# Performance work log

Hardware: AMD Instinct MI355X
Metric: run time of the kernel (lower is better)

The kernel has to match this reference:

```python
import jax, jax.numpy as jnp
import numpy as np

D_MODEL = 1024
NUM_HEADS = 16
D_K = D_MODEL // NUM_HEADS
B, L = 2, 4096


def setup_inputs() -> dict:
    key = jax.random.key(0)
    ks = jax.random.split(key, 12)
    s = 0.02
    return {
        "q": jax.random.normal(ks[0], (B, L, D_MODEL), dtype=jnp.float32),
        "k": jax.random.normal(ks[1], (B, L, D_MODEL), dtype=jnp.float32),
        "v": jax.random.normal(ks[2], (B, L, D_MODEL), dtype=jnp.float32),
        "Wq": jax.random.normal(ks[3], (D_MODEL, D_MODEL), dtype=jnp.float32) * s,
        "bq": jax.random.normal(ks[4], (D_MODEL,), dtype=jnp.float32) * s,
        "Wk": jax.random.normal(ks[5], (D_MODEL, D_MODEL), dtype=jnp.float32) * s,
        "bk": jax.random.normal(ks[6], (D_MODEL,), dtype=jnp.float32) * s,
        "Wv": jax.random.normal(ks[7], (D_MODEL, D_MODEL), dtype=jnp.float32) * s,
        "bv": jax.random.normal(ks[8], (D_MODEL,), dtype=jnp.float32) * s,
        "Wo": jax.random.normal(ks[9], (D_MODEL, D_MODEL), dtype=jnp.float32) * s,
        "bo": jax.random.normal(ks[10], (D_MODEL,), dtype=jnp.float32) * s,
    }


def reference(q, k, v, Wq, bq, Wk, bk, Wv, bv, Wo, bo):
    b, l, _ = q.shape
    # projections (torch Linear: x @ W.T + b), reshape to [b, l, h, d]
    qf = (q @ Wq.T + bq).reshape(b, l, NUM_HEADS, D_K)
    kf = (k @ Wk.T + bk).reshape(b, l, NUM_HEADS, D_K)
    vf = (v @ Wv.T + bv).reshape(b, l, NUM_HEADS, D_K)
    # elu+1 feature map (positive features)
    qf = jax.nn.elu(qf) + 1.0
    kf = jax.nn.elu(kf) + 1.0
    # normalizer uses full-sequence k sum (as in the original code)
    z = 1.0 / (jnp.einsum("blhd,bhd->blh", qf, kf.sum(axis=1)) + 1e-6)
    # cumulative sums over sequence (the linear-attention scan state)
    k_cum = jnp.cumsum(kf, axis=1)  # [b, l, h, d]
    v_cum = jnp.cumsum(vf, axis=1)  # [b, l, h, d]
    context = jnp.einsum("blhd,blhd->blh", qf, k_cum)  # [b, l, h]
    context = context[..., None] * v_cum * z[..., None]  # [b, l, h, d]
    context = context.reshape(b, l, NUM_HEADS * D_K)
    return context @ Wo.T + bo
```

## Files before the change

kernel.cpp:

```cpp
#include <hip/hip_runtime.h>
#include <hip/hip_bf16.h>
#include <cstdint>
#include <cstddef>

#define D_MODEL 1024
#define NUM_HEADS 16
#define DK_DIM 64
#define BATCH 2
#define SEQ 4096
#define MROWS (BATCH*SEQ)
#define NCHUNK 128
#define CHUNK 32

#define BM 256
#define BN 128
#define BK 64
#define NSLOT 3
#define SLOT_SH (BM*BK + BN*BK)
#define KTILES (D_MODEL/BK)

typedef __attribute__((ext_vector_type(4))) float f32x4;
typedef __attribute__((ext_vector_type(2))) float f32x2;
typedef __attribute__((ext_vector_type(8))) short bf16x8;
typedef __attribute__((ext_vector_type(4))) short s16x4;
typedef __attribute__((ext_vector_type(2))) uint32_t u32x2;
typedef __attribute__((ext_vector_type(4))) uint32_t u32x4;

__device__ __forceinline__ float b2f(short s) {
  union { uint32_t u; float f; } c; c.u = ((uint32_t)(uint16_t)s) << 16; return c.f;
}
__device__ __forceinline__ short f2b(float f) {
  union { float f; uint32_t u; } c; c.f = f;
  uint32_t u = c.u;
  u += 0x7FFFu + ((u >> 16) & 1u);
  return (short)(u >> 16);
}
__device__ __forceinline__ f32x4 b4_to_f4(s16x4 s) {
  f32x4 r;
  r.x = b2f(s.x); r.y = b2f(s.y); r.z = b2f(s.z); r.w = b2f(s.w);
  return r;
}
__device__ __forceinline__ uint32_t cvtpk(float lo, float hi) {
  uint32_t r;
  asm("v_cvt_pk_bf16_f32 %0, %1, %2" : "=v"(r) : "v"(lo), "v"(hi));
  return r;
}

__global__ __launch_bounds__(256) void cvt_w4(
    const float* __restrict__ s0, const float* __restrict__ s1,
    const float* __restrict__ s2, const float* __restrict__ s3,
    short* __restrict__ dst) {
  const int y = blockIdx.y;
  const float* s = (y == 0) ? s0 : (y == 1) ? s1 : (y == 2) ? s2 : s3;
  const int i = blockIdx.x * 256 + threadIdx.x;
  float4 v = reinterpret_cast<const float4*>(s)[i];
  s16x4 o;
  o.x = f2b(v.x); o.y = f2b(v.y); o.z = f2b(v.z); o.w = f2b(v.w);
  reinterpret_cast<s16x4*>(dst)[(size_t)y * (D_MODEL * D_MODEL / 4) + i] = o;
}

template<int AFP32, int OUTBF16, int CSUM>
__global__ __launch_bounds__(512, 2) void gemm8(
    const void* __restrict__ A0, const void* __restrict__ A1,
    const void* __restrict__ A2, const short* __restrict__ Wbase,
    const float* __restrict__ b0, const float* __restrict__ b1,
    const float* __restrict__ b2, void* __restrict__ Cbase, int actmask,
    float* __restrict__ ckp, float* __restrict__ cvp)
{
  extern __shared__ __align__(16) short lds[];
  const int tid = threadIdx.x;
  const int wid = tid >> 6;
  const int lane = tid & 63;
  const int brow = blockIdx.x * BM;
  const int bcol = blockIdx.y * BN;
  const int z = blockIdx.z;
  const int wr = wid >> 1, wc = wid & 1;

  const void* Ap = (z == 0) ? A0 : (z == 1) ? A1 : A2;
  const float* bias = (z == 0) ? b0 : (z == 1) ? b1 : b2;
  const short* Bw = Wbase + (size_t)z * D_MODEL * D_MODEL;
  const int act = (actmask >> z) & 1;
  const float* __restrict__ A32 = (const float*)Ap;
  const short* __restrict__ A16 = (const short*)Ap;

  f32x4 acc[4][4];
#pragma unroll
  for (int i = 0; i < 4; ++i)
#pragma unroll
    for (int j = 0; j < 4; ++j)
#pragma unroll
      for (int t = 0; t < 4; ++t) acc[i][j][t] = 0.f;

  const int srow = lane >> 3;
  const int gql  = lane & 7;
  const int sgel = (gql ^ srow) * 8;

  auto stageB = [&](int t) {
    short* sB = lds + (t % NSLOT) * SLOT_SH + BM * BK;
    const int k0 = t * BK;
#pragma unroll
    for (int i = 0; i < 2; ++i) {
      const int r = i * 64 + wid * 8;
      const short* g = Bw + (size_t)(bcol + r + srow) * D_MODEL + k0 + sgel;
      __builtin_amdgcn_global_load_lds((const __attribute__((address_space(1))) void*)g,
          (__attribute__((address_space(3))) void*)(sB + r * BK), 16, 0, 0);
    }
  };
  auto stageA16 = [&](int t) {
    short* sA = lds + (t % NSLOT) * SLOT_SH;
    const int k0 = t * BK;
#pragma unroll
    for (int i = 0; i < 4; ++i) {
      const int r = i * 64 + wid * 8;
      const short* g = A16 + (size_t)(brow + r + srow) * D_MODEL + k0 + sgel;
      __builtin_amdgcn_global_load_lds((const __attribute__((address_space(1))) void*)g,
          (__attribute__((address_space(3))) void*)(sA + r * BK), 16, 0, 0);
    }
  };
  auto loadA32 = [&](int t, float4 (&buf)[8]) {
    const int k0 = t * BK;
#pragma unroll
    for (int i = 0; i < 4; ++i) {
      const float* src = A32 + (size_t)(brow + i * 64 + wid * 8 + srow) * D_MODEL + k0 + gql * 8;
      buf[2 * i]     = *reinterpret_cast<const float4*>(src);
      buf[2 * i + 1] = *reinterpret_cast<const float4*>(src + 4);
    }
  };
  auto writeA32 = [&](int t, float4 (&buf)[8]) {
    char* sA = (char*)(lds + (t % NSLOT) * SLOT_SH);
#pragma unroll
    for (int i = 0; i < 4; ++i) {
      u32x4 w;
      w.x = cvtpk(buf[2 * i].x,     buf[2 * i].y);
      w.y = cvtpk(buf[2 * i].z,     buf[2 * i].w);
      w.z = cvtpk(buf[2 * i + 1].x, buf[2 * i + 1].y);
      w.w = cvtpk(buf[2 * i + 1].z, buf[2 * i + 1].w);
      const int ebyte = (i * 64 + wid * 8 + srow) * 128 + ((gql ^ srow) * 16);
      *reinterpret_cast<u32x4*>(sA + ebyte) = w;
    }
  };

  const int lane15 = lane & 15;
  const int swz = (lane & 7) << 4;
  const int kq = (lane >> 4) * 16;

  auto compute = [&](int t) {
    const char* sAb = (const char*)(lds + (t % NSLOT) * SLOT_SH);
    const char* sBb = sAb + BM * BK * 2;
    auto rdA = [&](int mi, int ks) -> bf16x8 {
      const int row = wr * 64 + mi * 16 + lane15;
      const int off = row * 128 + ((ks * 64 + kq) ^ swz);
      return *reinterpret_cast<const bf16x8*>(sAb + off);
    };
    auto rdB = [&](int nj, int ks) -> bf16x8 {
      const int row = wc * 64 + nj * 16 + lane15;
      const int off = row * 128 + ((ks * 64 + kq) ^ swz);
      return *reinterpret_cast<const bf16x8*>(sBb + off);
    };
    bf16x8 Af[2][2], Bf[2][2][2];
#pragma unroll
    for (int m2 = 0; m2 < 2; ++m2)
#pragma unroll
      for (int ks = 0; ks < 2; ++ks) Af[m2][ks] = rdA(m2, ks);
#pragma unroll
    for (int j2 = 0; j2 < 2; ++j2)
#pragma unroll
      for (int ks = 0; ks < 2; ++ks) Bf[0][j2][ks] = rdB(j2, ks);
#pragma unroll
    for (int m2 = 0; m2 < 2; ++m2)
#pragma unroll
      for (int j2 = 0; j2 < 2; ++j2)
#pragma unroll
        for (int ks = 0; ks < 2; ++ks)
          acc[m2][j2] = __builtin_amdgcn_mfma_f32_16x16x32_bf16(Bf[0][j2][ks], Af[m2][ks], acc[m2][j2], 0, 0, 0);
#pragma unroll
    for (int j2 = 0; j2 < 2; ++j2)
#pragma unroll
      for (int ks = 0; ks < 2; ++ks) Bf[1][j2][ks] = rdB(2 + j2, ks);
#pragma unroll
    for (int m2 = 0; m2 < 2; ++m2)
#pragma unroll
      for (int j2 = 0; j2 < 2; ++j2)
#pragma unroll
        for (int ks = 0; ks < 2; ++ks)
          acc[m2][2 + j2] = __builtin_amdgcn_mfma_f32_16x16x32_bf16(Bf[1][j2][ks], Af[m2][ks], acc[m2][2 + j2], 0, 0, 0);
#pragma unroll
    for (int m2 = 0; m2 < 2; ++m2)
#pragma unroll
      for (int ks = 0; ks < 2; ++ks) Af[m2][ks] = rdA(2 + m2, ks);
#pragma unroll
    for (int m2 = 0; m2 < 2; ++m2)
#pragma unroll
      for (int j2 = 0; j2 < 2; ++j2)
#pragma unroll
        for (int ks = 0; ks < 2; ++ks)
          acc[2 + m2][2 + j2] = __builtin_amdgcn_mfma_f32_16x16x32_bf16(Bf[1][j2][ks], Af[m2][ks], acc[2 + m2][2 + j2], 0, 0, 0);
#pragma unroll
    for (int m2 = 0; m2 < 2; ++m2)
#pragma unroll
      for (int j2 = 0; j2 < 2; ++j2)
#pragma unroll
        for (int ks = 0; ks < 2; ++ks)
          acc[2 + m2][j2] = __builtin_amdgcn_mfma_f32_16x16x32_bf16(Bf[0][j2][ks], Af[m2][ks], acc[2 + m2][j2], 0, 0, 0);
  };

  if constexpr (AFP32) {
    float4 buf0[8], buf1[8];
    loadA32(0, buf0);
    asm volatile("s_waitcnt vmcnt(0)" ::: "memory");
    writeA32(0, buf0);
    loadA32(1, buf1);
    stageB(0); stageB(1);

    auto body = [&](int t, float4 (&bufW)[8], float4 (&bufL)[8]) {
      if (t == KTILES - 1) { asm volatile("s_waitcnt vmcnt(0)" ::: "memory"); }
      else                 { asm volatile("s_waitcnt vmcnt(2)" ::: "memory"); }
      if (t + 1 < KTILES) writeA32(t + 1, bufW);
      if (t + 2 < KTILES) loadA32(t + 2, bufL);
      asm volatile("s_waitcnt lgkmcnt(0)" ::: "memory");
      __builtin_amdgcn_s_barrier();
      __builtin_amdgcn_sched_barrier(0);
      if (t + 2 < KTILES) stageB(t + 2);
      compute(t);
    };
#pragma unroll 1
    for (int t2 = 0; t2 < KTILES; t2 += 2) {
      body(t2,     buf1, buf0);
      body(t2 + 1, buf0, buf1);
    }
  } else {
    stageA16(0); stageB(0);
    stageA16(1); stageB(1);
#pragma unroll 1
    for (int t = 0; t < KTILES; ++t) {
      if (t == KTILES - 1) { asm volatile("s_waitcnt vmcnt(0)" ::: "memory"); }
      else                 { asm volatile("s_waitcnt vmcnt(6)" ::: "memory"); }
      __builtin_amdgcn_s_barrier();
      __builtin_amdgcn_sched_barrier(0);
      if (t + 2 < KTILES) { stageA16(t + 2); stageB(t + 2); }
      compute(t);
    }
  }

  const int csub4 = (lane >> 4) * 4;
  f32x4 csum[2][4];
  if constexpr (CSUM) {
#pragma unroll
    for (int cp = 0; cp < 2; ++cp)
#pragma unroll
      for (int nj = 0; nj < 4; ++nj)
#pragma unroll
        for (int t = 0; t < 4; ++t) csum[cp][nj][t] = 0.f;
  }
#pragma unroll
  for (int mi = 0; mi < 4; ++mi) {
    const int row = brow + wr * 64 + mi * 16 + lane15;
    const size_t rowbase = (size_t)z * MROWS * D_MODEL + (size_t)row * D_MODEL;
#pragma unroll
    for (int nj = 0; nj < 4; ++nj) {
      const int col0 = bcol + wc * 64 + nj * 16 + csub4;
      const float4 bv = *reinterpret_cast<const float4*>(&bias[col0]);
      float v0 = acc[mi][nj][0] + bv.x;
      float v1 = acc[mi][nj][1] + bv.y;
      float v2 = acc[mi][nj][2] + bv.z;
      float v3 = acc[mi][nj][3] + bv.w;
      if (act) {
        v0 = (v0 > 0.f) ? (v0 + 1.f) : __expf(v0);
        v1 = (v1 > 0.f) ? (v1 + 1.f) : __expf(v1);
        v2 = (v2 > 0.f) ? (v2 + 1.f) : __expf(v2);
        v3 = (v3 > 0.f) ? (v3 + 1.f) : __expf(v3);
      }
      if constexpr (CSUM) {
        csum[mi >> 1][nj][0] += v0;
        csum[mi >> 1][nj][1] += v1;
        csum[mi >> 1][nj][2] += v2;
        csum[mi >> 1][nj][3] += v3;
      }
      if (OUTBF16) {
        u32x2 w;
        w.x = cvtpk(v0, v1);
        w.y = cvtpk(v2, v3);
        *reinterpret_cast<u32x2*>(&((short*)Cbase)[rowbase + col0]) = w;
      } else {
        float4 w; w.x = v0; w.y = v1; w.z = v2; w.w = v3;
        *reinterpret_cast<float4*>(&((float*)Cbase)[rowbase + col0]) = w;
      }
    }
  }
  if constexpr (CSUM) {
    if (z >= 1) {
      float* dst = (z == 1) ? ckp : cvp;
      const int b  = brow >> 12;
      const int l0 = brow & (SEQ - 1);
      const int h  = (bcol >> 6) + wc;
      const int bh = b * NUM_HEADS + h;
#pragma unroll
      for (int cp = 0; cp < 2; ++cp) {
#pragma unroll
        for (int nj = 0; nj < 4; ++nj) {
          f32x4 s = csum[cp][nj];
#pragma unroll
          for (int m = 1; m < 16; m <<= 1) {
            s[0] += __shfl_xor(s[0], m, 64);
            s[1] += __shfl_xor(s[1], m, 64);
            s[2] += __shfl_xor(s[2], m, 64);
            s[3] += __shfl_xor(s[3], m, 64);
          }
          if (lane15 == 0) {
            const int cg = (l0 >> 5) + wr * 2 + cp;
            const int d0 = nj * 16 + csub4;
            *reinterpret_cast<f32x4*>(
                &dst[((size_t)(bh * NCHUNK + cg)) * DK_DIM + d0]) = s;
          }
        }
      }
    }
  }
}

__global__ __launch_bounds__(256) void chunk_scan(
    float* __restrict__ ck, float* __restrict__ cv, float* __restrict__ ksum)
{
  __shared__ float sk[4][64], sv[4][64];
  const int bh = blockIdx.x;
  const int tid = threadIdx.x;
  const int d = tid & 63;
  const int g = tid >> 6;
  const int c0 = g * 32;

  float rk = 0.f, rv = 0.f;
#pragma unroll 4
  for (int c = c0; c < c0 + 32; ++c) {
    const size_t o = ((size_t)(bh * NCHUNK + c)) * DK_DIM + d;
    rk += ck[o]; rv += cv[o];
  }
  sk[g][d] = rk; sv[g][d] = rv;
  __syncthreads();
  float runk = 0.f, runv = 0.f;
  for (int gg = 0; gg < g; ++gg) { runk += sk[gg][d]; runv += sv[gg][d]; }
#pragma unroll 4
  for (int c = c0; c < c0 + 32; ++c) {
    const size_t o = ((size_t)(bh * NCHUNK + c)) * DK_DIM + d;
    const float tk = ck[o], tv = cv[o];
    ck[o] = runk; cv[o] = runv;
    runk += tk; runv += tv;
  }
  if (g == 3) ksum[bh * DK_DIM + d] = runk;
}

__global__ __launch_bounds__(256) void scan_ctx(
    const short* __restrict__ qf, const short* __restrict__ kf,
    const short* __restrict__ vf,
    const float* __restrict__ ck, const float* __restrict__ cv,
    const float* __restrict__ ksum, short* __restrict__ ctx)
{
  const int gw = blockIdx.x * 4 + (threadIdx.x >> 6);
  const int lane = threadIdx.x & 63;
  const int pg = lane >> 4;
  const int dg = lane & 15;
  const int c = gw & (NCHUNK - 1);
  const int h = (gw >> 7) & (NUM_HEADS - 1);
  const int b = gw >> 11;
  const int bh = b * NUM_HEADS + h;
  const int d4 = dg * 4;

  f32x4 krun = *reinterpret_cast<const f32x4*>(
      &ck[((size_t)(bh * NCHUNK + c)) * DK_DIM + d4]);
  f32x4 vrun = *reinterpret_cast<const f32x4*>(
      &cv[((size_t)(bh * NCHUNK + c)) * DK_DIM + d4]);
  const f32x4 kst = *reinterpret_cast<const f32x4*>(&ksum[bh * DK_DIM + d4]);

  const size_t base = ((size_t)(b * SEQ + c * CHUNK) * NUM_HEADS + h) * DK_DIM + d4;

  for (int p0 = 0; p0 < CHUNK; p0 += 4) {
    const size_t qoff = base + (size_t)(p0 + pg) * D_MODEL;
    const f32x4 q4 = b4_to_f4(*reinterpret_cast<const s16x4*>(&qf[qoff]));
    f32x4 sk, sv;
#pragma unroll
    for (int i = 0; i < 4; ++i) {
      const size_t off = base + (size_t)(p0 + i) * D_MODEL;
      krun += b4_to_f4(*reinterpret_cast<const s16x4*>(&kf[off]));
      vrun += b4_to_f4(*reinterpret_cast<const s16x4*>(&vf[off]));
      if (i == pg) { sk = krun; sv = vrun; }
    }
    float s1 = q4.x * sk.x + q4.y * sk.y + q4.z * sk.z + q4.w * sk.w;
    float s2 = q4.x * kst.x + q4.y * kst.y + q4.z * kst.z + q4.w * kst.w;
#pragma unroll
    for (int m = 1; m < 16; m <<= 1) {
      s1 += __shfl_xor(s1, m, 64);
      s2 += __shfl_xor(s2, m, 64);
    }
    const float g = s1 / (s2 + 1e-6f);
    s16x4 o;
    o.x = f2b(g * sv.x); o.y = f2b(g * sv.y);
    o.z = f2b(g * sv.z); o.w = f2b(g * sv.w);
    *reinterpret_cast<s16x4*>(&ctx[qoff]) = o;
  }
}

extern "C" void kernel_launch(void* const* d_in, const int* in_sizes, int n_in,
                              void* d_out, int out_size, void* d_ws, size_t ws_size,
                              hipStream_t stream) {
  const float* q  = (const float*)d_in[0];
  const float* k  = (const float*)d_in[1];
  const float* v  = (const float*)d_in[2];
  const float* Wq = (const float*)d_in[3];
  const float* bq = (const float*)d_in[4];
  const float* Wk = (const float*)d_in[5];
  const float* bk = (const float*)d_in[6];
  const float* Wv = (const float*)d_in[7];
  const float* bv = (const float*)d_in[8];
  const float* Wo = (const float*)d_in[9];
  const float* bo = (const float*)d_in[10];
  float* out = (float*)d_out;

  uint8_t* p = (uint8_t*)d_ws;
  auto alloc = [&](size_t bytes) { uint8_t* r = p; p += bytes; return r; };
  short* qf  = (short*)alloc((size_t)MROWS * D_MODEL * 2);
  short* kf  = (short*)alloc((size_t)MROWS * D_MODEL * 2);
  short* vf  = (short*)alloc((size_t)MROWS * D_MODEL * 2);
  short* ctx = (short*)alloc((size_t)MROWS * D_MODEL * 2);
  short* Wqb = (short*)alloc((size_t)D_MODEL * D_MODEL * 2);
  short* Wkb = (short*)alloc((size_t)D_MODEL * D_MODEL * 2);
  short* Wvb = (short*)alloc((size_t)D_MODEL * D_MODEL * 2);
  short* Wob = (short*)alloc((size_t)D_MODEL * D_MODEL * 2);
  float* ck   = (float*)alloc((size_t)BATCH * NUM_HEADS * NCHUNK * DK_DIM * 4);
  float* cv   = (float*)alloc((size_t)BATCH * NUM_HEADS * NCHUNK * DK_DIM * 4);
  float* ksum = (float*)alloc((size_t)BATCH * NUM_HEADS * DK_DIM * 4);
  (void)Wkb; (void)Wvb;

  const dim3 gproj(MROWS / BM, D_MODEL / BN, 3);
  const dim3 gout (MROWS / BM, D_MODEL / BN, 1);
  const int shbytes = NSLOT * SLOT_SH * (int)sizeof(short);

  (void)hipFuncSetAttribute((const void*)gemm8<1, 1, 1>,
      hipFuncAttributeMaxDynamicSharedMemorySize, shbytes);
  (void)hipFuncSetAttribute((const void*)gemm8<0, 0, 0>,
      hipFuncAttributeMaxDynamicSharedMemorySize, shbytes);

  cvt_w4<<<dim3(D_MODEL * D_MODEL / 4 / 256, 4), 256, 0, stream>>>(Wq, Wk, Wv, Wo, Wqb);

  gemm8<1, 1, 1><<<gproj, 512, shbytes, stream>>>(q, k, v, Wqb, bq, bk, bv, qf, 0x3, ck, cv);

  chunk_scan<<<BATCH * NUM_HEADS, 256, 0, stream>>>(ck, cv, ksum);
  scan_ctx<<<BATCH * NUM_HEADS * NCHUNK / 4, 256, 0, stream>>>(qf, kf, vf, ck, cv, ksum, ctx);

  gemm8<0, 0, 0><<<gout, 512, shbytes, stream>>>(ctx, ctx, ctx, Wob, bo, bo, bo, out, 0, nullptr, nullptr);
}
```

Before: 136.5 us.

## Split projection GEMM into smaller 128x128 double-buffered kernel, keep out-GEMM separate

```diff
diff --git a/kernel.cpp b/kernel.cpp
--- a/kernel.cpp
+++ b/kernel.cpp
@@ -12,15 +12,17 @@
 #define NCHUNK 128
 #define CHUNK 32
 
-#define BM 256
+#define BM 128
 #define BN 128
 #define BK 64
-#define NSLOT 3
-#define SLOT_SH (BM*BK + BN*BK)
+#define SLOT_SH ((BM+BN)*BK)
 #define KTILES (D_MODEL/BK)
+#define OBM 256
+#define OBN 128
+#define ONSLOT 3
+#define OSLOT_SH (OBM*BK + OBN*BK)
 
 typedef __attribute__((ext_vector_type(4))) float f32x4;
-typedef __attribute__((ext_vector_type(2))) float f32x2;
 typedef __attribute__((ext_vector_type(8))) short bf16x8;
 typedef __attribute__((ext_vector_type(4))) short s16x4;
 typedef __attribute__((ext_vector_type(2))) uint32_t u32x2;
@@ -59,12 +61,11 @@
   reinterpret_cast<s16x4*>(dst)[(size_t)y * (D_MODEL * D_MODEL / 4) + i] = o;
 }
 
-template<int AFP32, int OUTBF16, int CSUM>
-__global__ __launch_bounds__(512, 2) void gemm8(
+__global__ __launch_bounds__(256, 2) void gemm_proj(
     const void* __restrict__ A0, const void* __restrict__ A1,
     const void* __restrict__ A2, const short* __restrict__ Wbase,
     const float* __restrict__ b0, const float* __restrict__ b1,
-    const float* __restrict__ b2, void* __restrict__ Cbase, int actmask,
+    const float* __restrict__ b2, short* __restrict__ Cbase, int actmask,
     float* __restrict__ ckp, float* __restrict__ cvp)
 {
   extern __shared__ __align__(16) short lds[];
@@ -76,12 +77,10 @@
   const int z = blockIdx.z;
   const int wr = wid >> 1, wc = wid & 1;
 
-  const void* Ap = (z == 0) ? A0 : (z == 1) ? A1 : A2;
+  const float* A32 = (const float*)((z == 0) ? A0 : (z == 1) ? A1 : A2);
   const float* bias = (z == 0) ? b0 : (z == 1) ? b1 : b2;
   const short* Bw = Wbase + (size_t)z * D_MODEL * D_MODEL;
   const int act = (actmask >> z) & 1;
-  const float* __restrict__ A32 = (const float*)Ap;
-  const short* __restrict__ A16 = (const short*)Ap;
 
   f32x4 acc[4][4];
 #pragma unroll
@@ -95,163 +94,100 @@
   const int gql  = lane & 7;
   const int sgel = (gql ^ srow) * 8;
 
-  auto stageB = [&](int t) {
-    short* sB = lds + (t % NSLOT) * SLOT_SH + BM * BK;
+  float4 abuf[8];
+
+  auto loadA = [&](int t) {
     const int k0 = t * BK;
 #pragma unroll
-    for (int i = 0; i < 2; ++i) {
-      const int r = i * 64 + wid * 8;
+    for (int i = 0; i < 4; ++i) {
+      const float* src = A32 + (size_t)(brow + i * 32 + wid * 8 + srow) * D_MODEL + k0 + gql * 8;
+      abuf[2 * i]     = *reinterpret_cast<const float4*>(src);
+      abuf[2 * i + 1] = *reinterpret_cast<const float4*>(src + 4);
+    }
+  };
+  auto writeA = [&](int slot) {
+    char* sA = (char*)(lds + slot * SLOT_SH);
+#pragma unroll
+    for (int i = 0; i < 4; ++i) {
+      u32x4 w;
+      w.x = cvtpk(abuf[2 * i].x,     abuf[2 * i].y);
+      w.y = cvtpk(abuf[2 * i].z,     abuf[2 * i].w);
+      w.z = cvtpk(abuf[2 * i + 1].x, abuf[2 * i + 1].y);
+      w.w = cvtpk(abuf[2 * i + 1].z, abuf[2 * i + 1].w);
+      const int ebyte = (i * 32 + wid * 8 + srow) * 128 + ((gql ^ srow) * 16);
+      *reinterpret_cast<u32x4*>(sA + ebyte) = w;
+    }
+  };
+  auto stageB = [&](int t, int slot) {
+    short* sB = lds + slot * SLOT_SH + BM * BK;
+    const int k0 = t * BK;
+#pragma unroll
+    for (int i = 0; i < 4; ++i) {
+      const int r = i * 32 + wid * 8;
       const short* g = Bw + (size_t)(bcol + r + srow) * D_MODEL + k0 + sgel;
       __builtin_amdgcn_global_load_lds((const __attribute__((address_space(1))) void*)g,
           (__attribute__((address_space(3))) void*)(sB + r * BK), 16, 0, 0);
     }
   };
-  auto stageA16 = [&](int t) {
-    short* sA = lds + (t % NSLOT) * SLOT_SH;
-    const int k0 = t * BK;
-#pragma unroll
-    for (int i = 0; i < 4; ++i) {
-      const int r = i * 64 + wid * 8;
-      const short* g = A16 + (size_t)(brow + r + srow) * D_MODEL + k0 + sgel;
-      __builtin_amdgcn_global_load_lds((const __attribute__((address_space(1))) void*)g,
-          (__attribute__((address_space(3))) void*)(sA + r * BK), 16, 0, 0);
-    }
-  };
-  auto loadA32 = [&](int t, float4 (&buf)[8]) {
-    const int k0 = t * BK;
-#pragma unroll
-    for (int i = 0; i < 4; ++i) {
-      const float* src = A32 + (size_t)(brow + i * 64 + wid * 8 + srow) * D_MODEL + k0 + gql * 8;
-      buf[2 * i]     = *reinterpret_cast<const float4*>(src);
-      buf[2 * i + 1] = *reinterpret_cast<const float4*>(src + 4);
-    }
-  };
-  auto writeA32 = [&](int t, float4 (&buf)[8]) {
-    char* sA = (char*)(lds + (t % NSLOT) * SLOT_SH);
-#pragma unroll
-    for (int i = 0; i < 4; ++i) {
-      u32x4 w;
-      w.x = cvtpk(buf[2 * i].x,     buf[2 * i].y);
-      w.y = cvtpk(buf[2 * i].z,     buf[2 * i].w);
-      w.z = cvtpk(buf[2 * i + 1].x, buf[2 * i + 1].y);
-      w.w = cvtpk(buf[2 * i + 1].z, buf[2 * i + 1].w);
-      const int ebyte = (i * 64 + wid * 8 + srow) * 128 + ((gql ^ srow) * 16);
-      *reinterpret_cast<u32x4*>(sA + ebyte) = w;
-    }
-  };
 
   const int lane15 = lane & 15;
   const int swz = (lane & 7) << 4;
   const int kq = (lane >> 4) * 16;
 
-  auto compute = [&](int t) {
-    const char* sAb = (const char*)(lds + (t % NSLOT) * SLOT_SH);
+  auto compute = [&](int slot) {
+    const char* sAb = (const char*)(lds + slot * SLOT_SH);
     const char* sBb = sAb + BM * BK * 2;
-    auto rdA = [&](int mi, int ks) -> bf16x8 {
-      const int row = wr * 64 + mi * 16 + lane15;
-      const int off = row * 128 + ((ks * 64 + kq) ^ swz);
-      return *reinterpret_cast<const bf16x8*>(sAb + off);
-    };
-    auto rdB = [&](int nj, int ks) -> bf16x8 {
-      const int row = wc * 64 + nj * 16 + lane15;
-      const int off = row * 128 + ((ks * 64 + kq) ^ swz);
-      return *reinterpret_cast<const bf16x8*>(sBb + off);
-    };
-    bf16x8 Af[2][2], Bf[2][2][2];
-#pragma unroll
-    for (int m2 = 0; m2 < 2; ++m2)
-#pragma unroll
-      for (int ks = 0; ks < 2; ++ks) Af[m2][ks] = rdA(m2, ks);
-#pragma unroll
-    for (int j2 = 0; j2 < 2; ++j2)
-#pragma unroll
-      for (int ks = 0; ks < 2; ++ks) Bf[0][j2][ks] = rdB(j2, ks);
-#pragma unroll
-    for (int m2 = 0; m2 < 2; ++m2)
-#pragma unroll
-      for (int j2 = 0; j2 < 2; ++j2)
-#pragma unroll
-        for (int ks = 0; ks < 2; ++ks)
-          acc[m2][j2] = __builtin_amdgcn_mfma_f32_16x16x32_bf16(Bf[0][j2][ks], Af[m2][ks], acc[m2][j2], 0, 0, 0);
-#pragma unroll
-    for (int j2 = 0; j2 < 2; ++j2)
-#pragma unroll
-      for (int ks = 0; ks < 2; ++ks) Bf[1][j2][ks] = rdB(2 + j2, ks);
-#pragma unroll
-    for (int m2 = 0; m2 < 2; ++m2)
-#pragma unroll
-      for (int j2 = 0; j2 < 2; ++j2)
-#pragma unroll
-        for (int ks = 0; ks < 2; ++ks)
-          acc[m2][2 + j2] = __builtin_amdgcn_mfma_f32_16x16x32_bf16(Bf[1][j2][ks], Af[m2][ks], acc[m2][2 + j2], 0, 0, 0);
-#pragma unroll
-    for (int m2 = 0; m2 < 2; ++m2)
-#pragma unroll
-      for (int ks = 0; ks < 2; ++ks) Af[m2][ks] = rdA(2 + m2, ks);
-#pragma unroll
-    for (int m2 = 0; m2 < 2; ++m2)
-#pragma unroll
-      for (int j2 = 0; j2 < 2; ++j2)
-#pragma unroll
-        for (int ks = 0; ks < 2; ++ks)
-          acc[2 + m2][2 + j2] = __builtin_amdgcn_mfma_f32_16x16x32_bf16(Bf[1][j2][ks], Af[m2][ks], acc[2 + m2][2 + j2], 0, 0, 0);
-#pragma unroll
-    for (int m2 = 0; m2 < 2; ++m2)
-#pragma unroll
-      for (int j2 = 0; j2 < 2; ++j2)
-#pragma unroll
-        for (int ks = 0; ks < 2; ++ks)
-          acc[2 + m2][j2] = __builtin_amdgcn_mfma_f32_16x16x32_bf16(Bf[0][j2][ks], Af[m2][ks], acc[2 + m2][j2], 0, 0, 0);
-  };
-
-  if constexpr (AFP32) {
-    float4 buf0[8], buf1[8];
-    loadA32(0, buf0);
-    asm volatile("s_waitcnt vmcnt(0)" ::: "memory");
-    writeA32(0, buf0);
-    loadA32(1, buf1);
-    stageB(0); stageB(1);
-
-    auto body = [&](int t, float4 (&bufW)[8], float4 (&bufL)[8]) {
-      if (t == KTILES - 1) { asm volatile("s_waitcnt vmcnt(0)" ::: "memory"); }
-      else                 { asm volatile("s_waitcnt vmcnt(2)" ::: "memory"); }
-      if (t + 1 < KTILES) writeA32(t + 1, bufW);
-      if (t + 2 < KTILES) loadA32(t + 2, bufL);
-      asm volatile("s_waitcnt lgkmcnt(0)" ::: "memory");
-      __builtin_amdgcn_s_barrier();
-      __builtin_amdgcn_sched_barrier(0);
-      if (t + 2 < KTILES) stageB(t + 2);
-      compute(t);
-    };
+#pragma unroll
+    for (int ks = 0; ks < 2; ++ks) {
+      bf16x8 Af[4], Bf[4];
+#pragma unroll
+      for (int mi = 0; mi < 4; ++mi)
+        Af[mi] = *reinterpret_cast<const bf16x8*>(
+            sAb + (wr * 64 + mi * 16 + lane15) * 128 + ((ks * 64 + kq) ^ swz));
+#pragma unroll
+      for (int nj = 0; nj < 4; ++nj)
+        Bf[nj] = *reinterpret_cast<const bf16x8*>(
+            sBb + (wc * 64 + nj * 16 + lane15) * 128 + ((ks * 64 + kq) ^ swz));
+#pragma unroll
+      for (int mi = 0; mi < 4; ++mi)
+#pragma unroll
+        for (int nj = 0; nj < 4; ++nj)
+          acc[mi][nj] = __builtin_amdgcn_mfma_f32_16x16x32_bf16(Bf[nj], Af[mi], acc[mi][nj], 0, 0, 0);
+    }
+  };
+
+  loadA(0);
+  asm volatile("s_waitcnt vmcnt(0)" ::: "memory");
+  writeA(0);
+  stageB(0, 0);
+  loadA(1);
+
 #pragma unroll 1
-    for (int t2 = 0; t2 < KTILES; t2 += 2) {
-      body(t2,     buf1, buf0);
-      body(t2 + 1, buf0, buf1);
-    }
-  } else {
-    stageA16(0); stageB(0);
-    stageA16(1); stageB(1);
-#pragma unroll 1
-    for (int t = 0; t < KTILES; ++t) {
-      if (t == KTILES - 1) { asm volatile("s_waitcnt vmcnt(0)" ::: "memory"); }
-      else                 { asm volatile("s_waitcnt vmcnt(6)" ::: "memory"); }
-      __builtin_amdgcn_s_barrier();
-      __builtin_amdgcn_sched_barrier(0);
-      if (t + 2 < KTILES) { stageA16(t + 2); stageB(t + 2); }
-      compute(t);
-    }
+  for (int t = 0; t < KTILES; ++t) {
+    const int cur = t & 1;
+    asm volatile("s_waitcnt lgkmcnt(0)" ::: "memory");
+    if (t == KTILES - 1) { asm volatile("s_waitcnt vmcnt(0)" ::: "memory"); }
+    else                 { asm volatile("s_waitcnt vmcnt(8)" ::: "memory"); }
+    __builtin_amdgcn_s_barrier();
+    __builtin_amdgcn_sched_barrier(0);
+    if (t + 1 < KTILES) {
+      stageB(t + 1, cur ^ 1);
+      asm volatile("s_waitcnt vmcnt(4)" ::: "memory");
+      writeA(cur ^ 1);
+      if (t + 2 < KTILES) loadA(t + 2);
+    }
+    compute(cur);
   }
 
   const int csub4 = (lane >> 4) * 4;
   f32x4 csum[2][4];
-  if constexpr (CSUM) {
-#pragma unroll
-    for (int cp = 0; cp < 2; ++cp)
-#pragma unroll
-      for (int nj = 0; nj < 4; ++nj)
-#pragma unroll
-        for (int t = 0; t < 4; ++t) csum[cp][nj][t] = 0.f;
-  }
+#pragma unroll
+  for (int cp = 0; cp < 2; ++cp)
+#pragma unroll
+    for (int nj = 0; nj < 4; ++nj)
+#pragma unroll
+      for (int t = 0; t < 4; ++t) csum[cp][nj][t] = 0.f;
+
 #pragma unroll
   for (int mi = 0; mi < 4; ++mi) {
     const int row = brow + wr * 64 + mi * 16 + lane15;
@@ -270,50 +206,181 @@
         v2 = (v2 > 0.f) ? (v2 + 1.f) : __expf(v2);
         v3 = (v3 > 0.f) ? (v3 + 1.f) : __expf(v3);
       }
-      if constexpr (CSUM) {
-        csum[mi >> 1][nj][0] += v0;
-        csum[mi >> 1][nj][1] += v1;
-        csum[mi >> 1][nj][2] += v2;
-        csum[mi >> 1][nj][3] += v3;
-      }
-      if (OUTBF16) {
-        u32x2 w;
-        w.x = cvtpk(v0, v1);
-        w.y = cvtpk(v2, v3);
-        *reinterpret_cast<u32x2*>(&((short*)Cbase)[rowbase + col0]) = w;
-      } else {
-        float4 w; w.x = v0; w.y = v1; w.z = v2; w.w = v3;
-        *reinterpret_cast<float4*>(&((float*)Cbase)[rowbase + col0]) = w;
-      }
-    }
-  }
-  if constexpr (CSUM) {
-    if (z >= 1) {
-      float* dst = (z == 1) ? ckp : cvp;
-      const int b  = brow >> 12;
-      const int l0 = brow & (SEQ - 1);
-      const int h  = (bcol >> 6) + wc;
-      const int bh = b * NUM_HEADS + h;
-#pragma unroll
-      for (int cp = 0; cp < 2; ++cp) {
-#pragma unroll
-        for (int nj = 0; nj < 4; ++nj) {
-          f32x4 s = csum[cp][nj];
-#pragma unroll
-          for (int m = 1; m < 16; m <<= 1) {
-            s[0] += __shfl_xor(s[0], m, 64);
-            s[1] += __shfl_xor(s[1], m, 64);
-            s[2] += __shfl_xor(s[2], m, 64);
-            s[3] += __shfl_xor(s[3], m, 64);
-          }
-          if (lane15 == 0) {
-            const int cg = (l0 >> 5) + wr * 2 + cp;
-            const int d0 = nj * 16 + csub4;
-            *reinterpret_cast<f32x4*>(
-                &dst[((size_t)(bh * NCHUNK + cg)) * DK_DIM + d0]) = s;
-          }
+      csum[mi >> 1][nj][0] += v0;
+      csum[mi >> 1][nj][1] += v1;
+      csum[mi >> 1][nj][2] += v2;
+      csum[mi >> 1][nj][3] += v3;
+      u32x2 w;
+      w.x = cvtpk(v0, v1);
+      w.y = cvtpk(v2, v3);
+      *reinterpret_cast<u32x2*>(&Cbase[rowbase + col0]) = w;
+    }
+  }
+  if (z >= 1) {
+    float* dst = (z == 1) ? ckp : cvp;
+    const int b  = brow >> 12;
+    const int l0 = brow & (SEQ - 1);
+    const int h  = (bcol >> 6) + wc;
+    const int bh = b * NUM_HEADS + h;
+#pragma unroll
+    for (int cp = 0; cp < 2; ++cp) {
+#pragma unroll
+      for (int nj = 0; nj < 4; ++nj) {
+        f32x4 s = csum[cp][nj];
+#pragma unroll
+        for (int m = 1; m < 16; m <<= 1) {
+          s[0] += __shfl_xor(s[0], m, 64);
+          s[1] += __shfl_xor(s[1], m, 64);
+          s[2] += __shfl_xor(s[2], m, 64);
+          s[3] += __shfl_xor(s[3], m, 64);
+        }
+        if (lane15 == 0) {
+          const int cg = (l0 >> 5) + wr * 2 + cp;
+          const int d0 = nj * 16 + csub4;
+          *reinterpret_cast<f32x4*>(
+              &dst[((size_t)(bh * NCHUNK + cg)) * DK_DIM + d0]) = s;
         }
       }
+    }
+  }
+}
+
+__global__ __launch_bounds__(512, 2) void gemm_out(
+    const short* __restrict__ A16, const short* __restrict__ Bw,
+    const float* __restrict__ bias, float* __restrict__ Cout)
+{
+  extern __shared__ __align__(16) short lds[];
+  const int tid = threadIdx.x;
+  const int wid = tid >> 6;
+  const int lane = tid & 63;
+  const int brow = blockIdx.x * OBM;
+  const int bcol = blockIdx.y * OBN;
+  const int wr = wid >> 1, wc = wid & 1;
+
+  f32x4 acc[4][4];
+#pragma unroll
+  for (int i = 0; i < 4; ++i)
+#pragma unroll
+    for (int j = 0; j < 4; ++j)
+#pragma unroll
+      for (int t = 0; t < 4; ++t) acc[i][j][t] = 0.f;
+
+  const int srow = lane >> 3;
+  const int gql  = lane & 7;
+  const int sgel = (gql ^ srow) * 8;
+
+  auto stageB = [&](int t) {
+    short* sB = lds + (t % ONSLOT) * OSLOT_SH + OBM * BK;
+    const int k0 = t * BK;
+#pragma unroll
+    for (int i = 0; i < 2; ++i) {
+      const int r = i * 64 + wid * 8;
+      const short* g = Bw + (size_t)(bcol + r + srow) * D_MODEL + k0 + sgel;
+      __builtin_amdgcn_global_load_lds((const __attribute__((address_space(1))) void*)g,
+          (__attribute__((address_space(3))) void*)(sB + r * BK), 16, 0, 0);
+    }
+  };
+  auto stageA = [&](int t) {
+    short* sA = lds + (t % ONSLOT) * OSLOT_SH;
+    const int k0 = t * BK;
+#pragma unroll
+    for (int i = 0; i < 4; ++i) {
+      const int r = i * 64 + wid * 8;
+      const short* g = A16 + (size_t)(brow + r + srow) * D_MODEL + k0 + sgel;
+      __builtin_amdgcn_global_load_lds((const __attribute__((address_space(1))) void*)g,
+          (__attribute__((address_space(3))) void*)(sA + r * BK), 16, 0, 0);
+    }
+  };
+
+  const int lane15 = lane & 15;
+  const int swz = (lane & 7) << 4;
+  const int kq = (lane >> 4) * 16;
+
+  auto compute = [&](int t) {
+    const char* sAb = (const char*)(lds + (t % ONSLOT) * OSLOT_SH);
+    const char* sBb = sAb + OBM * BK * 2;
+    auto rdA = [&](int mi, int ks) -> bf16x8 {
+      const int row = wr * 64 + mi * 16 + lane15;
+      return *reinterpret_cast<const bf16x8*>(sAb + row * 128 + ((ks * 64 + kq) ^ swz));
+    };
+    auto rdB = [&](int nj, int ks) -> bf16x8 {
+      const int row = wc * 64 + nj * 16 + lane15;
+      return *reinterpret_cast<const bf16x8*>(sBb + row * 128 + ((ks * 64 + kq) ^ swz));
+    };
+    bf16x8 Af[2][2], Bf[2][2][2];
+#pragma unroll
+    for (int m2 = 0; m2 < 2; ++m2)
+#pragma unroll
+      for (int ks = 0; ks < 2; ++ks) Af[m2][ks] = rdA(m2, ks);
+#pragma unroll
+    for (int j2 = 0; j2 < 2; ++j2)
+#pragma unroll
+      for (int ks = 0; ks < 2; ++ks) Bf[0][j2][ks] = rdB(j2, ks);
+#pragma unroll
+    for (int m2 = 0; m2 < 2; ++m2)
+#pragma unroll
+      for (int j2 = 0; j2 < 2; ++j2)
+#pragma unroll
+        for (int ks = 0; ks < 2; ++ks)
+          acc[m2][j2] = __builtin_amdgcn_mfma_f32_16x16x32_bf16(Bf[0][j2][ks], Af[m2][ks], acc[m2][j2], 0, 0, 0);
+#pragma unroll
+    for (int j2 = 0; j2 < 2; ++j2)
+#pragma unroll
+      for (int ks = 0; ks < 2; ++ks) Bf[1][j2][ks] = rdB(2 + j2, ks);
+#pragma unroll
+    for (int m2 = 0; m2 < 2; ++m2)
+#pragma unroll
+      for (int j2 = 0; j2 < 2; ++j2)
+#pragma unroll
+        for (int ks = 0; ks < 2; ++ks)
+          acc[m2][2 + j2] = __builtin_amdgcn_mfma_f32_16x16x32_bf16(Bf[1][j2][ks], Af[m2][ks], acc[m2][2 + j2], 0, 0, 0);
+#pragma unroll
+    for (int m2 = 0; m2 < 2; ++m2)
+#pragma unroll
+      for (int ks = 0; ks < 2; ++ks) Af[m2][ks] = rdA(2 + m2, ks);
+#pragma unroll
+    for (int m2 = 0; m2 < 2; ++m2)
+#pragma unroll
+      for (int j2 = 0; j2 < 2; ++j2)
+#pragma unroll
+        for (int ks = 0; ks < 2; ++ks)
+          acc[2 + m2][2 + j2] = __builtin_amdgcn_mfma_f32_16x16x32_bf16(Bf[1][j2][ks], Af[m2][ks], acc[2 + m2][2 + j2], 0, 0, 0);
+#pragma unroll
+    for (int m2 = 0; m2 < 2; ++m2)
+#pragma unroll
+      for (int j2 = 0; j2 < 2; ++j2)
+#pragma unroll
+        for (int ks = 0; ks < 2; ++ks)
+          acc[2 + m2][j2] = __builtin_amdgcn_mfma_f32_16x16x32_bf16(Bf[0][j2][ks], Af[m2][ks], acc[2 + m2][j2], 0, 0, 0);
+  };
+
+  stageA(0); stageB(0);
+  stageA(1); stageB(1);
+#pragma unroll 1
+  for (int t = 0; t < KTILES; ++t) {
+    if (t == KTILES - 1) { asm volatile("s_waitcnt vmcnt(0)" ::: "memory"); }
+    else                 { asm volatile("s_waitcnt vmcnt(6)" ::: "memory"); }
+    __builtin_amdgcn_s_barrier();
+    __builtin_amdgcn_sched_barrier(0);
+    if (t + 2 < KTILES) { stageA(t + 2); stageB(t + 2); }
+    compute(t);
+  }
+
+  const int csub4 = (lane >> 4) * 4;
+#pragma unroll
+  for (int mi = 0; mi < 4; ++mi) {
+    const int row = brow + wr * 64 + mi * 16 + lane15;
+    const size_t rowbase = (size_t)row * D_MODEL;
+#pragma unroll
+    for (int nj = 0; nj < 4; ++nj) {
+      const int col0 = bcol + wc * 64 + nj * 16 + csub4;
+      const float4 bv = *reinterpret_cast<const float4*>(&bias[col0]);
+      float4 w;
+      w.x = acc[mi][nj][0] + bv.x;
+      w.y = acc[mi][nj][1] + bv.y;
+      w.z = acc[mi][nj][2] + bv.z;
+      w.w = acc[mi][nj][3] + bv.w;
+      *reinterpret_cast<float4*>(&Cout[rowbase + col0]) = w;
     }
   }
 }
@@ -430,20 +497,21 @@
   (void)Wkb; (void)Wvb;
 
   const dim3 gproj(MROWS / BM, D_MODEL / BN, 3);
-  const dim3 gout (MROWS / BM, D_MODEL / BN, 1);
-  const int shbytes = NSLOT * SLOT_SH * (int)sizeof(short);
-
-  (void)hipFuncSetAttribute((const void*)gemm8<1, 1, 1>,
-      hipFuncAttributeMaxDynamicSharedMemorySize, shbytes);
-  (void)hipFuncSetAttribute((const void*)gemm8<0, 0, 0>,
-      hipFuncAttributeMaxDynamicSharedMemorySize, shbytes);
+  const dim3 gout (MROWS / OBM, D_MODEL / OBN, 1);
+  const int shproj = 2 * SLOT_SH * (int)sizeof(short);
+  const int shout  = ONSLOT * OSLOT_SH * (int)sizeof(short);
+
+  (void)hipFuncSetAttribute((const void*)gemm_proj,
+      hipFuncAttributeMaxDynamicSharedMemorySize, shproj);
+  (void)hipFuncSetAttribute((const void*)gemm_out,
+      hipFuncAttributeMaxDynamicSharedMemorySize, shout);
 
   cvt_w4<<<dim3(D_MODEL * D_MODEL / 4 / 256, 4), 256, 0, stream>>>(Wq, Wk, Wv, Wo, Wqb);
 
-  gemm8<1, 1, 1><<<gproj, 512, shbytes, stream>>>(q, k, v, Wqb, bq, bk, bv, qf, 0x3, ck, cv);
+  gemm_proj<<<gproj, 256, shproj, stream>>>(q, k, v, Wqb, bq, bk, bv, qf, 0x3, ck, cv);
 
   chunk_scan<<<BATCH * NUM_HEADS, 256, 0, stream>>>(ck, cv, ksum);
   scan_ctx<<<BATCH * NUM_HEADS * NCHUNK / 4, 256, 0, stream>>>(qf, kf, vf, ck, cv, ksum, ctx);
 
-  gemm8<0, 0, 0><<<gout, 512, shbytes, stream>>>(ctx, ctx, ctx, Wob, bo, bo, bo, out, 0, nullptr, nullptr);
-}
+  gemm_out<<<gout, 512, shout, stream>>>(ctx, Wob, bo, out);
+}
```

Result: slower. 141.9 us (+3.9%).
